# Optimization experiments

Measured on AMD Instinct MI355X. Metric: run time of the kernel, lower is better.

## Reference

```python
import jax, jax.numpy as jnp
import numpy as np
from jax.scipy.special import i0

B, P = 2, 524288
N = (512, 512)            # uniform frequency grid
M = 4                     # window cutoff m (2M taps per dim)
SIGMA = 2.0
NGRID = tuple(2 * (int(SIGMA * Ni) // 2) for Ni in N)  # oversampled grid (1024, 1024)
BETA = tuple(float(np.pi * (2.0 - 1.0 / (ng / Ni))) for ng, Ni in zip(NGRID, N))


def _phi_hat_1d(Ni, ni, b):
    # Fourier coefficients of the Kaiser-Bessel window, k = -Ni/2 .. Ni/2-1
    k = jnp.arange(-Ni // 2, Ni // 2, dtype=jnp.float32)
    arg = jnp.sqrt(b * b - (2.0 * jnp.pi * k / ni) ** 2)
    return i0(M * arg) / ni


def _window_ft():
    # separable d-dim Fourier coefficient grid, shape [N1, N2] (== window.ft)
    c1 = _phi_hat_1d(N[0], NGRID[0], BETA[0])
    c2 = _phi_hat_1d(N[1], NGRID[1], BETA[1])
    return c1[:, None] * c2[None, :]


def _phi(t, ni, b):
    # Kaiser-Bessel window in time domain, support |t| <= M/ni
    u2 = M * M - (ni * t) ** 2
    u = jnp.sqrt(jnp.maximum(u2, 1e-12))
    return jnp.where(u2 > 0, jnp.sinh(b * u) / (jnp.pi * u), 0.0)


def setup_inputs() -> dict:
    key = jax.random.key(0)
    k1, k2 = jax.random.split(key)
    x = jax.random.uniform(k1, (B, P, 2), jnp.float32, -0.5, 0.5)  # points on torus
    f_hat = jax.random.normal(k2, (B, N[0], N[1], 2), jnp.float32)  # complex as [re,im]
    return {"x": x, "f_hat": f_hat}


def _nfft_forward(x, f_hat):
    # f(x_j) ~= sum_k f_hat[k] exp(-2 pi i <k, x_j>) via window-deconvolved oversampled FFT + local gather
    fh = (f_hat[..., 0] + 1j * f_hat[..., 1]).astype(jnp.complex64)  # [B, N1, N2]
    ft = _window_ft().astype(jnp.float32)
    gh = fh / ft                                                    # deconvolve
    p1 = (NGRID[0] - N[0]) // 2
    p2 = (NGRID[1] - N[1]) // 2
    gh = jnp.pad(gh, ((0, 0), (p1, p1), (p2, p2)))                  # centered zero-pad to n
    g = jnp.fft.fftn(jnp.fft.ifftshift(gh, axes=(-2, -1)), axes=(-2, -1))
    g = g / (NGRID[0] * NGRID[1])                                   # g_l = (1/n) sum_k gh_k e^{-2pi i kl/n}

    offs = jnp.arange(-M + 1, M + 1)                                # [2M]
    ws, idxs = [], []
    for d in range(2):
        nd = NGRID[d]
        xd = x[..., d]                                              # [B, P]
        l0 = jnp.floor(xd * nd).astype(jnp.int32)
        l = l0[..., None] + offs                                    # [B, P, 2M]
        t = xd[..., None] - l.astype(jnp.float32) / nd
        ws.append(_phi(t, nd, BETA[d]))
        idxs.append(jnp.mod(l, nd))

    g_flat = g.reshape(B, NGRID[0] * NGRID[1])
    acc = jnp.zeros((B, P), jnp.complex64)
    for i in range(2 * M):                                          # fixed 2m x 2m taps
        for j in range(2 * M):
            flat = idxs[0][..., i] * NGRID[1] + idxs[1][..., j]     # [B, P]
            gv = jnp.take_along_axis(g_flat, flat, axis=1)
            acc = acc + (ws[0][..., i] * ws[1][..., j]) * gv
    return jnp.stack([acc.real, acc.imag], axis=-1)                 # [B, P, 2]


def reference(x, f_hat):
    return _nfft_forward(x, f_hat)
```

## Files before the change

kernel.cpp:

```cpp
#include <hip/hip_runtime.h>

constexpr int   BATCH = 2;
constexpr int   NPTS  = 524288;
constexpr int   BINS  = 2048;
constexpr int   CAP   = 768;
constexpr float BETA  = 4.71238898038469f;
constexpr float PI_F  = 3.14159265358979f;

#define PIDX(i) ((i) + ((i) >> 4))

constexpr size_t G_BYTES  = (size_t)BATCH * 1024 * 1024 * sizeof(float2);
constexpr size_t GCNT_OFF = G_BYTES;
constexpr size_t PERM_OFF = G_BYTES + 8192;

__device__ __forceinline__ float i0f_large(float x) {
    float t = 3.75f / x;
    float p =  0.00392377f;
    p = p * t + -0.01647633f;
    p = p * t +  0.02635537f;
    p = p * t + -0.02057706f;
    p = p * t +  0.00916281f;
    p = p * t + -0.00157565f;
    p = p * t +  0.00225319f;
    p = p * t +  0.01328592f;
    p = p * t +  0.39894228f;
    return __expf(x) * rsqrtf(x) * p;
}

__device__ __forceinline__ int tile_of(float2 xv, int b) {
    int c1 = ((int)floorf(xv.x * 1024.0f)) & 1023;
    int c2 = ((int)floorf(xv.y * 1024.0f)) & 1023;
    return (b << 10) + ((c1 >> 5) << 5) + (c2 >> 5);
}

__device__ __forceinline__ float2 cmul(float2 a, float2 w) {
    return make_float2(a.x * w.x - a.y * w.y, a.x * w.y + a.y * w.x);
}

__device__ __forceinline__ int digitrev4_10(int f) {
    unsigned r = __brev((unsigned)f) >> 22;
    return (int)(((r & 0x2AAu) >> 1) | ((r & 0x155u) << 1));
}

__device__ __forceinline__ void build_tw4(float2* T, int tid, int nthreads) {
    int off = 0, q = 256, sig = 1;
    #pragma unroll
    for (int st = 0; st < 5; ++st) {
        for (int m = tid; m < 3 * q; m += nthreads) {
            int sec = 0, j = m;
            if (j >= q) { sec++; j -= q; }
            if (j >= q) { sec++; j -= q; }
            float ang = (-2.0f * PI_F / 1024.0f) * (float)((sec + 1) * j * sig);
            float sw, cw;
            __sincosf(ang, &sw, &cw);
            T[off + m] = make_float2(cw, sw);
        }
        off += 3 * q; q >>= 2; sig <<= 2;
    }
}

__device__ __forceinline__ void bfly4(float2* s, const float2* T,
                                      int bt, int q, int off) {
    int j    = bt & (q - 1);
    int base = ((bt - j) << 2) + j;
    int p0 = PIDX(base), p1 = PIDX(base + q);
    int p2 = PIDX(base + 2 * q), p3 = PIDX(base + 3 * q);
    float2 a0 = s[p0], a1 = s[p1], a2 = s[p2], a3 = s[p3];
    float2 t0 = make_float2(a0.x + a2.x, a0.y + a2.y);
    float2 t1 = make_float2(a0.x - a2.x, a0.y - a2.y);
    float2 t2 = make_float2(a1.x + a3.x, a1.y + a3.y);
    float2 t3 = make_float2(a1.x - a3.x, a1.y - a3.y);
    float2 b0 = make_float2(t0.x + t2.x, t0.y + t2.y);
    float2 b2 = make_float2(t0.x - t2.x, t0.y - t2.y);
    float2 b1 = make_float2(t1.x + t3.y, t1.y - t3.x);
    float2 b3 = make_float2(t1.x - t3.y, t1.y + t3.x);
    s[p0] = b0;
    s[p1] = cmul(b1, T[off + j]);
    s[p2] = cmul(b2, T[off + q + j]);
    s[p3] = cmul(b3, T[off + 2 * q + j]);
}

__global__ __launch_bounds__(256) void rows_and_bin(const float2* __restrict__ fh,
                                                    float2* __restrict__ g,
                                                    const float2* __restrict__ x,
                                                    int* __restrict__ gcnt,
                                                    float4* __restrict__ perm) {
    __shared__ __align__(16) char smem[16880];
    int tid = threadIdx.x;

    if (blockIdx.x < 1024) {
        if (blockIdx.x == 0) {
            #pragma unroll
            for (int i = 0; i < 8; ++i)
                atomicExch(&gcnt[tid * 8 + i], 0);
        }
        float2* s = (float2*)smem;
        float2* T = (float2*)smem + 1087;
        int blk = blockIdx.x & 511;
        int b   = blockIdx.x >> 9;
        int row = (blk < 256) ? blk : blk + 512;
        int a1  = (row + 256) & 1023;

        build_tw4(T, tid, 256);

        float k1 = (float)(a1 - 256);
        float w1 = (2.0f * PI_F / 1024.0f) * k1;
        float c1 = i0f_large(4.0f * sqrtf(BETA * BETA - w1 * w1));

        const float2* fr = fh + ((long)b << 18) + ((long)a1 << 9);

        float w2a = (2.0f * PI_F / 1024.0f) * (float)tid;
        float c2a = i0f_large(4.0f * sqrtf(BETA * BETA - w2a * w2a));
        float w2b = (2.0f * PI_F / 1024.0f) * (float)(tid - 256);
        float c2b = i0f_large(4.0f * sqrtf(BETA * BETA - w2b * w2b));

        float2 va = fr[tid + 256];
        float2 vb = fr[tid];
        float ia = 1.0f / (c1 * c2a);
        float ib = 1.0f / (c1 * c2b);
        float2 A = make_float2(va.x * ia, va.y * ia);
        float2 B = make_float2(vb.x * ib, vb.y * ib);

        __syncthreads();

        s[PIDX(tid)]       = make_float2(A.x + B.x, A.y + B.y);
        s[PIDX(tid + 256)] = cmul(make_float2(A.x - B.y, A.y + B.x), T[tid]);
        s[PIDX(tid + 512)] = cmul(make_float2(A.x - B.x, A.y - B.y), T[256 + tid]);
        s[PIDX(tid + 768)] = cmul(make_float2(A.x + B.y, A.y - B.x), T[512 + tid]);

        int off = 768, q = 64;
        #pragma unroll
        for (int st = 0; st < 4; ++st) {
            __syncthreads();
            bfly4(s, T, tid, q, off);
            off += 3 * q; q >>= 2;
        }
        __syncthreads();

        float2* base = g + ((long)b << 20) + ((long)row << 10);
        #pragma unroll
        for (int i = 0; i < 4; ++i) {
            int idx = tid + (i << 8);
            base[idx] = s[PIDX(digitrev4_10(idx))];
        }
    } else {
        int* h = (int*)smem;
        int bblk = blockIdx.x - 1024;
        for (int i = tid; i < BINS; i += 256) h[i] = 0;
        __syncthreads();

        int base = bblk * 4096;
        int    tile[16];
        float2 pv[16];
        #pragma unroll
        for (int i = 0; i < 16; ++i) {
            int gid = base + tid + i * 256;
            pv[i]   = x[gid];
            tile[i] = tile_of(pv[i], gid >> 19);
            atomicAdd(&h[tile[i]], 1);
        }
        __syncthreads();

        #pragma unroll
        for (int j = 0; j < 8; ++j) {
            int bi = tid + j * 256;
            int c  = h[bi];
            h[bi]  = c ? atomicAdd(&gcnt[bi], c) : 0;
        }
        __syncthreads();

        #pragma unroll
        for (int i = 0; i < 16; ++i) {
            int gid = base + tid + i * 256;
            int pos = atomicAdd(&h[tile[i]], 1);
            perm[tile[i] * CAP + pos] =
                make_float4(pv[i].x, pv[i].y, __int_as_float(gid), 0.0f);
        }
    }
}

__global__ __launch_bounds__(256) void fft_cols(float2* __restrict__ g) {
    constexpr int STR = 1092;
    __shared__ float2 s[4 * STR];
    __shared__ float2 T[1023];
    int b  = blockIdx.y;
    int C0 = blockIdx.x * 4;
    int t  = threadIdx.x;
    int c  = t & 3, L = t >> 2;
    float2* gb = g + ((long)b << 20);

    build_tw4(T, t, 256);

    float2 E[16];
    #pragma unroll
    for (int m = 0; m < 4; ++m) {
        int r = L + 64 * m;
        E[m] = gb[((long)r << 10) + C0 + c];
    }
    #pragma unroll
    for (int m = 12; m < 16; ++m) {
        int r = L + 64 * m;
        E[m] = gb[((long)r << 10) + C0 + c];
    }
    __syncthreads();

    #pragma unroll
    for (int m = 0; m < 4; ++m) {
        float2 A = E[m], B = E[m + 12];
        int j = L + 64 * m;
        E[m]      = make_float2(A.x + B.x, A.y + B.y);
        E[m + 4]  = cmul(make_float2(A.x - B.y, A.y + B.x), T[j]);
        E[m + 8]  = cmul(make_float2(A.x - B.x, A.y - B.y), T[256 + j]);
        E[m + 12] = cmul(make_float2(A.x + B.y, A.y - B.x), T[512 + j]);
    }

    {
        float2 u1 = T[768 + L], u2 = T[768 + 64 + L], u3 = T[768 + 128 + L];
        #pragma unroll
        for (int a = 0; a < 4; ++a) {
            float2 a0 = E[4*a], a1 = E[4*a+1], a2 = E[4*a+2], a3 = E[4*a+3];
            float2 t0 = make_float2(a0.x + a2.x, a0.y + a2.y);
            float2 t1 = make_float2(a0.x - a2.x, a0.y - a2.y);
            float2 t2 = make_float2(a1.x + a3.x, a1.y + a3.y);
            float2 t3 = make_float2(a1.x - a3.x, a1.y - a3.y);
            E[4*a]   = make_float2(t0.x + t2.x, t0.y + t2.y);
            E[4*a+1] = cmul(make_float2(t1.x + t3.y, t1.y - t3.x), u1);
            E[4*a+2] = cmul(make_float2(t0.x - t2.x, t0.y - t2.y), u2);
            E[4*a+3] = cmul(make_float2(t1.x - t3.y, t1.y + t3.x), u3);
        }
    }

    float2* sf = s + c * STR;
    #pragma unroll
    for (int m = 0; m < 16; ++m) sf[PIDX(L + 64 * m)] = E[m];

    int off = 960, q = 16;
    #pragma unroll
    for (int st = 0; st < 3; ++st) {
        __syncthreads();
        #pragma unroll
        for (int rr = 0; rr < 4; ++rr)
            bfly4(sf, T, L + rr * 64, q, off);
        off += 3 * q; q >>= 2;
    }
    __syncthreads();

    #pragma unroll
    for (int i = 0; i < 16; ++i) {
        int r = L + i * 64;
        gb[((long)r << 10) + C0 + c] = sf[PIDX(digitrev4_10(r))];
    }
}

__global__ __launch_bounds__(256) void gather_binned(const float2* __restrict__ g,
                                                     const int* __restrict__ gcnt,
                                                     const float4* __restrict__ perm,
                                                     float2* __restrict__ out) {
    __shared__ float2 patch[37 * 37];
    int tb = blockIdx.x;
    int b  = tb >> 10;
    int tt = tb & 1023;
    int tR = tt >> 5, tC = tt & 31;
    int R0 = (tR << 5) - 2, C0 = (tC << 5) - 2;
    const float2* gb = g + ((long)b << 20);

    for (int p = threadIdx.x; p < 37 * 37; p += 256) {
        int pr = p / 37, pc = p - pr * 37;
        int gr = (R0 + pr) & 1023, gc = (C0 + pc) & 1023;
        patch[p] = gb[(gr << 10) + gc];
    }
    __syncthreads();

    int cnt = gcnt[tb];
    if (cnt > CAP) cnt = CAP;
    int off0 = tb * CAP;
    for (int i = (int)threadIdx.x; i < cnt; i += 256) {
        float4 rec = perm[off0 + i];
        int gid = __float_as_int(rec.z);

        float w1[6], w2[6];
        int rr0, cc0;
        {
            float xs = rec.x * 1024.0f;
            float fl = floorf(xs);
            float fr = xs - fl;
            rr0 = (((int)fl) & 1023) - (tR << 5);
            #pragma unroll
            for (int k = 0; k < 6; ++k) {
                float tv = fr - (float)(k - 2);
                float u2 = 16.0f - tv * tv;
                float ir = rsqrtf(u2);
                float z  = BETA * u2 * ir;
                w1[k] = __expf(z) * 0.159154943f * ir;
            }
        }
        {
            float xs = rec.y * 1024.0f;
            float fl = floorf(xs);
            float fr = xs - fl;
            cc0 = (((int)fl) & 1023) - (tC << 5);
            #pragma unroll
            for (int k = 0; k < 6; ++k) {
                float tv = fr - (float)(k - 2);
                float u2 = 16.0f - tv * tv;
                float ir = rsqrtf(u2);
                float z  = BETA * u2 * ir;
                w2[k] = __expf(z) * 0.159154943f * ir;
            }
        }

        float ar = 0.0f, ai = 0.0f;
        #pragma unroll
        for (int ii = 0; ii < 6; ++ii) {
            int pbase = (rr0 + ii) * 37 + cc0;
            float wi = w1[ii];
            #pragma unroll
            for (int jj = 0; jj < 6; ++jj) {
                float2 gv = patch[pbase + jj];
                float w = wi * w2[jj];
                ar = fmaf(w, gv.x, ar);
                ai = fmaf(w, gv.y, ai);
            }
        }
        out[gid] = make_float2(ar, ai);
    }
}

extern "C" void kernel_launch(void* const* d_in, const int* in_sizes, int n_in,
                              void* d_out, int out_size, void* d_ws, size_t ws_size,
                              hipStream_t stream) {
    const float2* x  = (const float2*)d_in[0];
    const float2* fh = (const float2*)d_in[1];
    char* ws = (char*)d_ws;
    float2* g    = (float2*)ws;
    int*    gcnt = (int*)(ws + GCNT_OFF);
    float4* perm = (float4*)(ws + PERM_OFF);

    rows_and_bin<<<dim3(1280), dim3(256), 0, stream>>>(fh, g, x, gcnt, perm);
    fft_cols    <<<dim3(256, BATCH), dim3(256), 0, stream>>>(g);

    gather_binned<<<dim3(BINS), dim3(256), 0, stream>>>(g, gcnt, perm, (float2*)d_out);
}
```

Measured before the change: 117.1 us.

## Vectorize complex math with packed float2 and finish column FFT in registers

Complex arithmetic now uses ext_vector_type(2), and twiddles are stored as float4 (cos, sin, -sin, cos), so complex multiplies can map onto packed FMA instructions on CDNA. In the column FFT, the last two radix-4 stages run in registers after one shared-memory transpose instead of going through shared-memory butterflies, which removes two barriers and their LDS traffic. The cost is a doubled twiddle table in LDS, which raises shared-memory use and may lower occupancy, plus more register pressure from holding 16 values per thread in the column kernel.

```diff
diff --git a/kernel.cpp b/kernel.cpp
--- a/kernel.cpp
+++ b/kernel.cpp
@@ -7,9 +7,11 @@
 constexpr float BETA  = 4.71238898038469f;
 constexpr float PI_F  = 3.14159265358979f;
 
+typedef float v2f __attribute__((ext_vector_type(2)));
+
 #define PIDX(i) ((i) + ((i) >> 4))
 
-constexpr size_t G_BYTES  = (size_t)BATCH * 1024 * 1024 * sizeof(float2);
+constexpr size_t G_BYTES  = (size_t)BATCH * 1024 * 1024 * sizeof(v2f);
 constexpr size_t GCNT_OFF = G_BYTES;
 constexpr size_t PERM_OFF = G_BYTES + 8192;
 
@@ -27,22 +29,24 @@
     return __expf(x) * rsqrtf(x) * p;
 }
 
-__device__ __forceinline__ int tile_of(float2 xv, int b) {
+__device__ __forceinline__ int tile_of(v2f xv, int b) {
     int c1 = ((int)floorf(xv.x * 1024.0f)) & 1023;
     int c2 = ((int)floorf(xv.y * 1024.0f)) & 1023;
     return (b << 10) + ((c1 >> 5) << 5) + (c2 >> 5);
 }
 
-__device__ __forceinline__ float2 cmul(float2 a, float2 w) {
-    return make_float2(a.x * w.x - a.y * w.y, a.x * w.y + a.y * w.x);
-}
+__device__ __forceinline__ v2f cmul4(v2f a, float4 t) {
+    v2f lo = {t.x, t.y}, hi = {t.z, t.w};
+    return a.x * lo + a.y * hi;
+}
+__device__ __forceinline__ v2f irot(v2f b) { return (v2f){-b.y, b.x}; }
 
 __device__ __forceinline__ int digitrev4_10(int f) {
     unsigned r = __brev((unsigned)f) >> 22;
     return (int)(((r & 0x2AAu) >> 1) | ((r & 0x155u) << 1));
 }
 
-__device__ __forceinline__ void build_tw4(float2* T, int tid, int nthreads) {
+__device__ __forceinline__ void build_tw4(float4* T, int tid, int nthreads) {
     int off = 0, q = 256, sig = 1;
     #pragma unroll
     for (int st = 0; st < 5; ++st) {
@@ -53,39 +57,33 @@
             float ang = (-2.0f * PI_F / 1024.0f) * (float)((sec + 1) * j * sig);
             float sw, cw;
             __sincosf(ang, &sw, &cw);
-            T[off + m] = make_float2(cw, sw);
+            T[off + m] = make_float4(cw, sw, -sw, cw);
         }
         off += 3 * q; q >>= 2; sig <<= 2;
     }
 }
 
-__device__ __forceinline__ void bfly4(float2* s, const float2* T,
+__device__ __forceinline__ void bfly4(v2f* s, const float4* T,
                                       int bt, int q, int off) {
     int j    = bt & (q - 1);
     int base = ((bt - j) << 2) + j;
     int p0 = PIDX(base), p1 = PIDX(base + q);
     int p2 = PIDX(base + 2 * q), p3 = PIDX(base + 3 * q);
-    float2 a0 = s[p0], a1 = s[p1], a2 = s[p2], a3 = s[p3];
-    float2 t0 = make_float2(a0.x + a2.x, a0.y + a2.y);
-    float2 t1 = make_float2(a0.x - a2.x, a0.y - a2.y);
-    float2 t2 = make_float2(a1.x + a3.x, a1.y + a3.y);
-    float2 t3 = make_float2(a1.x - a3.x, a1.y - a3.y);
-    float2 b0 = make_float2(t0.x + t2.x, t0.y + t2.y);
-    float2 b2 = make_float2(t0.x - t2.x, t0.y - t2.y);
-    float2 b1 = make_float2(t1.x + t3.y, t1.y - t3.x);
-    float2 b3 = make_float2(t1.x - t3.y, t1.y + t3.x);
-    s[p0] = b0;
-    s[p1] = cmul(b1, T[off + j]);
-    s[p2] = cmul(b2, T[off + q + j]);
-    s[p3] = cmul(b3, T[off + 2 * q + j]);
-}
-
-__global__ __launch_bounds__(256) void rows_and_bin(const float2* __restrict__ fh,
-                                                    float2* __restrict__ g,
-                                                    const float2* __restrict__ x,
+    v2f a0 = s[p0], a1 = s[p1], a2 = s[p2], a3 = s[p3];
+    v2f t0 = a0 + a2, t1 = a0 - a2, t2 = a1 + a3, t3 = a1 - a3;
+    v2f r3 = irot(t3);
+    s[p0] = t0 + t2;
+    s[p1] = cmul4(t1 - r3, T[off + j]);
+    s[p2] = cmul4(t0 - t2, T[off + q + j]);
+    s[p3] = cmul4(t1 + r3, T[off + 2 * q + j]);
+}
+
+__global__ __launch_bounds__(256) void rows_and_bin(const v2f* __restrict__ fh,
+                                                    v2f* __restrict__ g,
+                                                    const v2f* __restrict__ x,
                                                     int* __restrict__ gcnt,
                                                     float4* __restrict__ perm) {
-    __shared__ __align__(16) char smem[16880];
+    __shared__ __align__(16) char smem[25072];
     int tid = threadIdx.x;
 
     if (blockIdx.x < 1024) {
@@ -94,8 +92,8 @@
             for (int i = 0; i < 8; ++i)
                 atomicExch(&gcnt[tid * 8 + i], 0);
         }
-        float2* s = (float2*)smem;
-        float2* T = (float2*)smem + 1087;
+        v2f*    s = (v2f*)smem;
+        float4* T = (float4*)(smem + 8704);
         int blk = blockIdx.x & 511;
         int b   = blockIdx.x >> 9;
         int row = (blk < 256) ? blk : blk + 512;
@@ -107,26 +105,23 @@
         float w1 = (2.0f * PI_F / 1024.0f) * k1;
         float c1 = i0f_large(4.0f * sqrtf(BETA * BETA - w1 * w1));
 
-        const float2* fr = fh + ((long)b << 18) + ((long)a1 << 9);
+        const v2f* fr = fh + ((long)b << 18) + ((long)a1 << 9);
 
         float w2a = (2.0f * PI_F / 1024.0f) * (float)tid;
         float c2a = i0f_large(4.0f * sqrtf(BETA * BETA - w2a * w2a));
         float w2b = (2.0f * PI_F / 1024.0f) * (float)(tid - 256);
         float c2b = i0f_large(4.0f * sqrtf(BETA * BETA - w2b * w2b));
 
-        float2 va = fr[tid + 256];
-        float2 vb = fr[tid];
-        float ia = 1.0f / (c1 * c2a);
-        float ib = 1.0f / (c1 * c2b);
-        float2 A = make_float2(va.x * ia, va.y * ia);
-        float2 B = make_float2(vb.x * ib, vb.y * ib);
-
-        __syncthreads();
-
-        s[PIDX(tid)]       = make_float2(A.x + B.x, A.y + B.y);
-        s[PIDX(tid + 256)] = cmul(make_float2(A.x - B.y, A.y + B.x), T[tid]);
-        s[PIDX(tid + 512)] = cmul(make_float2(A.x - B.x, A.y - B.y), T[256 + tid]);
-        s[PIDX(tid + 768)] = cmul(make_float2(A.x + B.y, A.y - B.x), T[512 + tid]);
+        v2f A = fr[tid + 256] * (1.0f / (c1 * c2a));
+        v2f B = fr[tid]       * (1.0f / (c1 * c2b));
+
+        __syncthreads();
+
+        v2f rB = irot(B);
+        s[PIDX(tid)]       = A + B;
+        s[PIDX(tid + 256)] = cmul4(A + rB, T[tid]);
+        s[PIDX(tid + 512)] = cmul4(A - B,  T[256 + tid]);
+        s[PIDX(tid + 768)] = cmul4(A - rB, T[512 + tid]);
 
         int off = 768, q = 64;
         #pragma unroll
@@ -137,7 +132,7 @@
         }
         __syncthreads();
 
-        float2* base = g + ((long)b << 20) + ((long)row << 10);
+        v2f* base = g + ((long)b << 20) + ((long)row << 10);
         #pragma unroll
         for (int i = 0; i < 4; ++i) {
             int idx = tid + (i << 8);
@@ -150,8 +145,8 @@
         __syncthreads();
 
         int base = bblk * 4096;
-        int    tile[16];
-        float2 pv[16];
+        int tile[16];
+        v2f pv[16];
         #pragma unroll
         for (int i = 0; i < 16; ++i) {
             int gid = base + tid + i * 256;
@@ -179,19 +174,19 @@
     }
 }
 
-__global__ __launch_bounds__(256) void fft_cols(float2* __restrict__ g) {
+__global__ __launch_bounds__(256) void fft_cols(v2f* __restrict__ g) {
     constexpr int STR = 1092;
-    __shared__ float2 s[4 * STR];
-    __shared__ float2 T[1023];
+    __shared__ v2f    s[4 * STR];
+    __shared__ float4 T[1023];
     int b  = blockIdx.y;
     int C0 = blockIdx.x * 4;
     int t  = threadIdx.x;
     int c  = t & 3, L = t >> 2;
-    float2* gb = g + ((long)b << 20);
+    v2f* gb = g + ((long)b << 20);
 
     build_tw4(T, t, 256);
 
-    float2 E[16];
+    v2f E[16];
     #pragma unroll
     for (int m = 0; m < 4; ++m) {
         int r = L + 64 * m;
@@ -206,63 +201,83 @@
 
     #pragma unroll
     for (int m = 0; m < 4; ++m) {
-        float2 A = E[m], B = E[m + 12];
+        v2f A = E[m], B = E[m + 12];
+        v2f rB = irot(B);
         int j = L + 64 * m;
-        E[m]      = make_float2(A.x + B.x, A.y + B.y);
-        E[m + 4]  = cmul(make_float2(A.x - B.y, A.y + B.x), T[j]);
-        E[m + 8]  = cmul(make_float2(A.x - B.x, A.y - B.y), T[256 + j]);
-        E[m + 12] = cmul(make_float2(A.x + B.y, A.y - B.x), T[512 + j]);
+        E[m]      = A + B;
+        E[m + 4]  = cmul4(A + rB, T[j]);
+        E[m + 8]  = cmul4(A - B,  T[256 + j]);
+        E[m + 12] = cmul4(A - rB, T[512 + j]);
     }
 
     {
-        float2 u1 = T[768 + L], u2 = T[768 + 64 + L], u3 = T[768 + 128 + L];
+        float4 u1 = T[768 + L], u2 = T[768 + 64 + L], u3 = T[768 + 128 + L];
         #pragma unroll
         for (int a = 0; a < 4; ++a) {
-            float2 a0 = E[4*a], a1 = E[4*a+1], a2 = E[4*a+2], a3 = E[4*a+3];
-            float2 t0 = make_float2(a0.x + a2.x, a0.y + a2.y);
-            float2 t1 = make_float2(a0.x - a2.x, a0.y - a2.y);
-            float2 t2 = make_float2(a1.x + a3.x, a1.y + a3.y);
-            float2 t3 = make_float2(a1.x - a3.x, a1.y - a3.y);
-            E[4*a]   = make_float2(t0.x + t2.x, t0.y + t2.y);
-            E[4*a+1] = cmul(make_float2(t1.x + t3.y, t1.y - t3.x), u1);
-            E[4*a+2] = cmul(make_float2(t0.x - t2.x, t0.y - t2.y), u2);
-            E[4*a+3] = cmul(make_float2(t1.x - t3.y, t1.y + t3.x), u3);
-        }
-    }
-
-    float2* sf = s + c * STR;
+            v2f a0 = E[4*a], a1 = E[4*a+1], a2 = E[4*a+2], a3 = E[4*a+3];
+            v2f t0 = a0 + a2, t1 = a0 - a2, t2 = a1 + a3, t3 = a1 - a3;
+            v2f r3 = irot(t3);
+            E[4*a]   = t0 + t2;
+            E[4*a+1] = cmul4(t1 - r3, u1);
+            E[4*a+2] = cmul4(t0 - t2, u2);
+            E[4*a+3] = cmul4(t1 + r3, u3);
+        }
+    }
+
+    v2f* sf = s + c * STR;
     #pragma unroll
     for (int m = 0; m < 16; ++m) sf[PIDX(L + 64 * m)] = E[m];
-
-    int off = 960, q = 16;
-    #pragma unroll
-    for (int st = 0; st < 3; ++st) {
-        __syncthreads();
-        #pragma unroll
-        for (int rr = 0; rr < 4; ++rr)
-            bfly4(sf, T, L + rr * 64, q, off);
-        off += 3 * q; q >>= 2;
-    }
     __syncthreads();
 
     #pragma unroll
-    for (int i = 0; i < 16; ++i) {
-        int r = L + i * 64;
-        gb[((long)r << 10) + C0 + c] = sf[PIDX(digitrev4_10(r))];
-    }
-}
-
-__global__ __launch_bounds__(256) void gather_binned(const float2* __restrict__ g,
+    for (int rr = 0; rr < 4; ++rr)
+        bfly4(sf, T, L + rr * 64, 16, 960);
+    __syncthreads();
+
+    v2f C[16];
+    int cb = 17 * L;
+    #pragma unroll
+    for (int j = 0; j < 16; ++j) C[j] = sf[cb + j];
+
+    #pragma unroll
+    for (int j = 0; j < 4; ++j) {
+        v2f a0 = C[j], a1 = C[j+4], a2 = C[j+8], a3 = C[j+12];
+        v2f t0 = a0 + a2, t1 = a0 - a2, t2 = a1 + a3, t3 = a1 - a3;
+        v2f r3 = irot(t3);
+        C[j]    = t0 + t2;
+        C[j+4]  = cmul4(t1 - r3, T[1008 + j]);
+        C[j+8]  = cmul4(t0 - t2, T[1012 + j]);
+        C[j+12] = cmul4(t1 + r3, T[1016 + j]);
+    }
+    #pragma unroll
+    for (int e = 0; e < 4; ++e) {
+        v2f a0 = C[4*e], a1 = C[4*e+1], a2 = C[4*e+2], a3 = C[4*e+3];
+        v2f t0 = a0 + a2, t1 = a0 - a2, t2 = a1 + a3, t3 = a1 - a3;
+        v2f r3 = irot(t3);
+        C[4*e]   = t0 + t2;
+        C[4*e+1] = t1 - r3;
+        C[4*e+2] = t0 - t2;
+        C[4*e+3] = t1 + r3;
+    }
+
+    #pragma unroll
+    for (int j = 0; j < 16; ++j) {
+        int r = digitrev4_10((L << 4) + j);
+        gb[((long)r << 10) + C0 + c] = C[j];
+    }
+}
+
+__global__ __launch_bounds__(256) void gather_binned(const v2f* __restrict__ g,
                                                      const int* __restrict__ gcnt,
                                                      const float4* __restrict__ perm,
-                                                     float2* __restrict__ out) {
-    __shared__ float2 patch[37 * 37];
+                                                     v2f* __restrict__ out) {
+    __shared__ v2f patch[37 * 37];
     int tb = blockIdx.x;
     int b  = tb >> 10;
     int tt = tb & 1023;
     int tR = tt >> 5, tC = tt & 31;
     int R0 = (tR << 5) - 2, C0 = (tC << 5) - 2;
-    const float2* gb = g + ((long)b << 20);
+    const v2f* gb = g + ((long)b << 20);
 
     for (int p = threadIdx.x; p < 37 * 37; p += 256) {
         int pr = p / 37, pc = p - pr * 37;
@@ -309,35 +324,31 @@
             }
         }
 
-        float ar = 0.0f, ai = 0.0f;
+        v2f acc = {0.0f, 0.0f};
         #pragma unroll
         for (int ii = 0; ii < 6; ++ii) {
             int pbase = (rr0 + ii) * 37 + cc0;
             float wi = w1[ii];
             #pragma unroll
-            for (int jj = 0; jj < 6; ++jj) {
-                float2 gv = patch[pbase + jj];
-                float w = wi * w2[jj];
-                ar = fmaf(w, gv.x, ar);
-                ai = fmaf(w, gv.y, ai);
-            }
-        }
-        out[gid] = make_float2(ar, ai);
+            for (int jj = 0; jj < 6; ++jj)
+                acc += (wi * w2[jj]) * patch[pbase + jj];
+        }
+        out[gid] = acc;
     }
 }
 
 extern "C" void kernel_launch(void* const* d_in, const int* in_sizes, int n_in,
                               void* d_out, int out_size, void* d_ws, size_t ws_size,
                               hipStream_t stream) {
-    const float2* x  = (const float2*)d_in[0];
-    const float2* fh = (const float2*)d_in[1];
+    const v2f* x  = (const v2f*)d_in[0];
+    const v2f* fh = (const v2f*)d_in[1];
     char* ws = (char*)d_ws;
-    float2* g    = (float2*)ws;
+    v2f*    g    = (v2f*)ws;
     int*    gcnt = (int*)(ws + GCNT_OFF);
     float4* perm = (float4*)(ws + PERM_OFF);
 
     rows_and_bin<<<dim3(1280), dim3(256), 0, stream>>>(fh, g, x, gcnt, perm);
     fft_cols    <<<dim3(256, BATCH), dim3(256), 0, stream>>>(g);
 
-    gather_binned<<<dim3(BINS), dim3(256), 0, stream>>>(g, gcnt, perm, (float2*)d_out);
-}
+    gather_binned<<<dim3(BINS), dim3(256), 0, stream>>>(g, gcnt, perm, (v2f*)d_out);
+}
```

Result: no change. 115.5 us, median of 2 (-1.4%).
